# Kernel optimization log

Measured on AMD Instinct MI355X. Metric: run time of the kernel, lower is better.

## Reference

```python
import jax, jax.numpy as jnp
import numpy as np

NUM_NODES = 100000
NUM_EDGES = 1200000
DIM = 64
NUM_LAYERS = 3
NUM_GRAPHS = 512
BN_EPS = 1e-5


def setup_inputs() -> dict:
    key = jax.random.key(0)
    ks = jax.random.split(key, 12)
    x = jax.random.normal(ks[0], (NUM_NODES, DIM), dtype=jnp.float32)
    edge_index = jax.random.randint(ks[1], (2, NUM_EDGES), 0, NUM_NODES, dtype=jnp.int64)
    edge_weight = jax.random.uniform(ks[2], (NUM_EDGES,), dtype=jnp.float32)
    batch = jnp.sort(jax.random.randint(ks[3], (NUM_NODES,), 0, NUM_GRAPHS, dtype=jnp.int64))
    W1 = jax.random.normal(ks[4], (NUM_LAYERS, DIM, DIM), dtype=jnp.float32) * 0.1
    b1 = jax.random.normal(ks[5], (NUM_LAYERS, DIM), dtype=jnp.float32) * 0.1
    W2 = jax.random.normal(ks[6], (NUM_LAYERS, DIM, DIM), dtype=jnp.float32) * 0.1
    b2 = jax.random.normal(ks[7], (NUM_LAYERS, DIM), dtype=jnp.float32) * 0.1
    gamma = jax.random.uniform(ks[8], (NUM_LAYERS, DIM), dtype=jnp.float32) + 0.5
    beta = jax.random.normal(ks[9], (NUM_LAYERS, DIM), dtype=jnp.float32) * 0.1
    return {"x": x, "edge_index": edge_index, "edge_weight": edge_weight,
            "batch": batch, "pool": 0, "W1": W1, "b1": b1, "W2": W2,
            "b2": b2, "gamma": gamma, "beta": beta}


def reference(x, edge_index, edge_weight, batch, pool, W1, b1, W2, b2, gamma, beta):
    # WGINConv (eps=0): h = MLP(x + scatter_add(edge_weight * x[src] -> dst))
    # then ReLU, then BatchNorm1d in training mode (batch statistics).
    src, dst = edge_index[0], edge_index[1]
    n_nodes = x.shape[0]
    xs = []
    for i in range(W1.shape[0]):
        msg = x[src] * edge_weight[:, None]                       # [E, D] gather
        agg = jax.ops.segment_sum(msg, dst, num_segments=n_nodes)  # [N, D] scatter-add
        h = agg + x                                                # (1+eps)*x, eps=0
        h = jax.nn.relu(h @ W1[i].T + b1[i]) @ W2[i].T + b2[i]     # GIN MLP
        h = jax.nn.relu(h)
        mu = h.mean(0)
        var = ((h - mu) ** 2).mean(0)                              # biased var (BN train)
        x = gamma[i] * (h - mu) * jax.lax.rsqrt(var + BN_EPS) + beta[i]
        xs.append(x)
    if pool == 0:  # 'add' pooling (static python int)
        xpool = [jax.ops.segment_sum(v, batch, num_segments=NUM_GRAPHS) for v in xs]
    else:          # 'mean' pooling
        counts = jax.ops.segment_sum(jnp.ones((n_nodes,), x.dtype), batch,
                                     num_segments=NUM_GRAPHS)
        denom = jnp.maximum(counts, 1.0)[:, None]
        xpool = [jax.ops.segment_sum(v, batch, num_segments=NUM_GRAPHS) / denom for v in xs]
    return (jnp.concatenate(xpool, axis=1), jnp.concatenate(xs, axis=1))
```

## Files before the change

kernel.cpp:

```cpp
#include <hip/hip_runtime.h>

#define N_NODES 100000
#define N_EDGES 1200000
#define DIM     64
#define N_LAYERS 3
#define N_GRAPHS 512
#define OUTD    192
#define BN_EPS  1e-5f

#define ELL_CAP 48

#define SCAN_CHUNK 1024
#define NBLK ((N_NODES + SCAN_CHUNK - 1) / SCAN_CHUNK)

#define NPB 64
#define LDS_PITCH 65
#define NLBLK ((N_NODES + NPB - 1) / NPB)

__global__ void transpose_w(const float* __restrict__ W1, const float* __restrict__ W2,
                            float* __restrict__ W1T, float* __restrict__ W2T,
                            float* __restrict__ idaff) {
    int idx = blockIdx.x * blockDim.x + threadIdx.x;
    if (idx < 128) idaff[idx] = (idx < 64) ? 1.0f : 0.0f;
    if (idx >= N_LAYERS * DIM * DIM) return;
    int l = idx >> 12;
    int r = idx & 4095;
    int j = r >> 6;
    int k = r & 63;
    int dstp = (l << 12) + k * DIM + j;
    W1T[dstp] = W1[idx];
    W2T[dstp] = W2[idx];
}

__global__ void edge_bin_ell(const int* __restrict__ src, const int* __restrict__ dst,
                             const float* __restrict__ ew,
                             int* __restrict__ cursor, int2* __restrict__ pe) {
    int e = blockIdx.x * blockDim.x + threadIdx.x;
    if (e >= N_EDGES) return;
    int t = dst[e];
    int pos = atomicAdd(&cursor[t], 1);
    if (pos < ELL_CAP)
        pe[(size_t)t * ELL_CAP + pos] = make_int2(src[e], __float_as_int(ew[e]));
}

__global__ void hist_kernel(const int* __restrict__ dst, int* __restrict__ counts) {
    int e = blockIdx.x * blockDim.x + threadIdx.x;
    if (e >= N_EDGES) return;
    atomicAdd(&counts[dst[e]], 1);
}

__global__ void scan_partial(const int* __restrict__ C, int* __restrict__ bsum) {
    __shared__ int lds[256];
    int b = blockIdx.x, t = threadIdx.x;
    int base = b * SCAN_CHUNK + t * 4;
    int s = 0;
#pragma unroll
    for (int k = 0; k < 4; ++k) {
        int i = base + k;
        if (i < N_NODES) s += C[i];
    }
    lds[t] = s;
    __syncthreads();
    for (int o = 128; o > 0; o >>= 1) {
        if (t < o) lds[t] += lds[t + o];
        __syncthreads();
    }
    if (t == 0) bsum[b] = lds[0];
}

__global__ void scan_bsum(int* __restrict__ bsum) {
    __shared__ int lds[128];
    int t = threadIdx.x;
    int v = (t < NBLK) ? bsum[t] : 0;
    lds[t] = v;
    __syncthreads();
    for (int o = 1; o < 128; o <<= 1) {
        int add = (t >= o) ? lds[t - o] : 0;
        __syncthreads();
        lds[t] += add;
        __syncthreads();
    }
    if (t < NBLK) bsum[t] = lds[t] - v;
}

__global__ void scan_final(const int* __restrict__ C, const int* __restrict__ bsum,
                           int* __restrict__ O, int* __restrict__ cursor) {
    __shared__ int lds[256];
    int b = blockIdx.x, t = threadIdx.x;
    int base = b * SCAN_CHUNK + t * 4;
    int v[4];
    int s = 0;
#pragma unroll
    for (int k = 0; k < 4; ++k) {
        int i = base + k;
        v[k] = (i < N_NODES) ? C[i] : 0;
        s += v[k];
    }
    lds[t] = s;
    __syncthreads();
    for (int o = 1; o < 256; o <<= 1) {
        int add = (t >= o) ? lds[t - o] : 0;
        __syncthreads();
        lds[t] += add;
        __syncthreads();
    }
    int off = bsum[b] + (lds[t] - s);
#pragma unroll
    for (int k = 0; k < 4; ++k) {
        int i = base + k;
        if (i < N_NODES) {
            O[i] = off;
            cursor[i] = off;
            off += v[k];
            if (i == N_NODES - 1) O[N_NODES] = off;
        }
    }
}

__global__ void edge_bin_csr(const int* __restrict__ src, const int* __restrict__ dst,
                             const float* __restrict__ ew,
                             int* __restrict__ cursor, int2* __restrict__ pe) {
    int e = blockIdx.x * blockDim.x + threadIdx.x;
    if (e >= N_EDGES) return;
    int t = dst[e];
    int pos = atomicAdd(&cursor[t], 1);
    pe[pos] = make_int2(src[e], __float_as_int(ew[e]));
}

template <bool ELL>
__global__ void __launch_bounds__(256) layer_kernel(
    const float* __restrict__ x_in, int xstride,
    const int* __restrict__ seg,
    const int2* __restrict__ pe,
    const float* __restrict__ affine ,
    const float* __restrict__ W1T, const float* __restrict__ b1,
    const float* __restrict__ W2T, const float* __restrict__ b2,
    float* __restrict__ out ,
    float* __restrict__ pstat ) {
    __shared__ float lds[NPB * LDS_PITCH];
    int t = threadIdx.x;
    int lane = t & 63;
    int wid = __builtin_amdgcn_readfirstlane(t >> 6);
    int nbase = blockIdx.x * NPB;

    float sc_in = affine[lane];
    float sh_in = affine[64 + lane];

    for (int nn = 0; nn < 16; ++nn) {
        int n = nbase + wid * 16 + nn;
        float acc = 0.0f;
        if (n < N_NODES) {
            int beg, end;
            if (ELL) { beg = n * ELL_CAP; end = beg + seg[n]; }
            else     { beg = seg[n];      end = seg[n + 1]; }
            float a0 = x_in[(size_t)n * xstride + lane];
            float a1 = 0.0f, a2 = 0.0f, a3 = 0.0f;
            float ws = 0.0f;
            int e = beg;
            for (; e + 4 <= end; e += 4) {
                int2 p0 = pe[e];
                int2 p1 = pe[e + 1];
                int2 p2 = pe[e + 2];
                int2 p3 = pe[e + 3];
                float w0 = __int_as_float(p0.y);
                float w1 = __int_as_float(p1.y);
                float w2 = __int_as_float(p2.y);
                float w3 = __int_as_float(p3.y);
                a0 = fmaf(w0, x_in[(size_t)p0.x * xstride + lane], a0);
                a1 = fmaf(w1, x_in[(size_t)p1.x * xstride + lane], a1);
                a2 = fmaf(w2, x_in[(size_t)p2.x * xstride + lane], a2);
                a3 = fmaf(w3, x_in[(size_t)p3.x * xstride + lane], a3);
                ws += (w0 + w1) + (w2 + w3);
            }
            for (; e < end; ++e) {
                int2 p = pe[e];
                float w = __int_as_float(p.y);
                a1 = fmaf(w, x_in[(size_t)p.x * xstride + lane], a1);
                ws += w;
            }
            acc = fmaf(sc_in, (a0 + a1) + (a2 + a3), sh_in * (1.0f + ws));
        }
        lds[(wid * 16 + nn) * LDS_PITCH + lane] = acc;
    }
    __syncthreads();

    float h[16];
#pragma unroll
    for (int jj = 0; jj < 16; ++jj) h[jj] = b1[wid * 16 + jj];
#pragma unroll 4
    for (int k = 0; k < DIM; ++k) {
        float xv = lds[lane * LDS_PITCH + k];
        const float* wr = W1T + k * DIM + wid * 16;
#pragma unroll
        for (int jj = 0; jj < 16; ++jj) h[jj] = fmaf(xv, wr[jj], h[jj]);
    }
#pragma unroll
    for (int jj = 0; jj < 16; ++jj) h[jj] = fmaxf(h[jj], 0.0f);
    __syncthreads();
#pragma unroll
    for (int jj = 0; jj < 16; ++jj) lds[lane * LDS_PITCH + wid * 16 + jj] = h[jj];
    __syncthreads();

    float o[16];
#pragma unroll
    for (int jj = 0; jj < 16; ++jj) o[jj] = b2[wid * 16 + jj];
#pragma unroll 4
    for (int k = 0; k < DIM; ++k) {
        float hv = lds[lane * LDS_PITCH + k];
        const float* wr = W2T + k * DIM + wid * 16;
#pragma unroll
        for (int jj = 0; jj < 16; ++jj) o[jj] = fmaf(hv, wr[jj], o[jj]);
    }
    int n = nbase + lane;
    bool valid = (n < N_NODES);
#pragma unroll
    for (int jj = 0; jj < 16; ++jj) o[jj] = fmaxf(o[jj], 0.0f);
    if (valid) {
        float* orow = out + (size_t)n * OUTD + wid * 16;
#pragma unroll
        for (int jj = 0; jj < 16; jj += 4) {
            *(float4*)(orow + jj) = make_float4(o[jj], o[jj + 1], o[jj + 2], o[jj + 3]);
        }
    }

    float my_s = 0.0f, my_q = 0.0f;
#pragma unroll
    for (int jj = 0; jj < 16; ++jj) {
        float v = valid ? o[jj] : 0.0f;
        float vs = v, vq = v * v;
#pragma unroll
        for (int m = 1; m < 64; m <<= 1) {
            vs += __shfl_xor(vs, m);
            vq += __shfl_xor(vq, m);
        }
        if (lane == jj) { my_s = vs; my_q = vq; }
    }
    if (lane < 16) {
        size_t base = (size_t)blockIdx.x * 128 + wid * 16 + lane;
        pstat[base] = my_s;
        pstat[base + 64] = my_q;
    }
}

__global__ void __launch_bounds__(256) reduce_stats(
    const float* __restrict__ pstat,
    const float* __restrict__ gamma, const float* __restrict__ beta,
    float* __restrict__ ss ) {
    __shared__ double part[16][16];
    int b = blockIdx.x;
    int t = threadIdx.x;
    int slot = t & 15;
    int g = t >> 4;
    int d = b * 8 + (slot & 7);
    int off = (slot < 8) ? 0 : 64;
    double s = 0.0;
    for (int blk = g; blk < NLBLK; blk += 16)
        s += (double)pstat[(size_t)blk * 128 + off + d];
    part[g][slot] = s;
    __syncthreads();
    if (t < 16) {
        double x = 0.0;
#pragma unroll
        for (int k = 0; k < 16; ++k) x += part[k][t];
        part[0][t] = x;
    }
    __syncthreads();
    if (t < 8) {
        int dd = b * 8 + t;
        double mu = part[0][t] / (double)N_NODES;
        double var = part[0][8 + t] / (double)N_NODES - mu * mu;
        float inv = (float)(1.0 / sqrt(var + (double)BN_EPS));
        float sc = gamma[dd] * inv;
        ss[dd] = sc;
        ss[64 + dd] = beta[dd] - (float)mu * sc;
    }
}

__global__ void bn_pool(float* __restrict__ xs,
                        const int* __restrict__ batch,
                        const float* __restrict__ ss ,
                        float* __restrict__ pooled) {
    int g = blockIdx.x;
    int part = blockIdx.y;
    int d = threadIdx.x;
    int l = d >> 6, dd = d & 63;
    float sc = ss[l * 128 + dd];
    float sh = ss[l * 128 + 64 + dd];
    int start, end;
    {
        int lo = 0, hi = N_NODES;
        while (lo < hi) { int m = (lo + hi) >> 1; if (batch[m] < g) lo = m + 1; else hi = m; }
        start = lo;
    }
    {
        int lo = start, hi = N_NODES;
        while (lo < hi) { int m = (lo + hi) >> 1; if (batch[m] <= g) lo = m + 1; else hi = m; }
        end = lo;
    }
    float acc = 0.0f;
    for (int n = start + part; n < end; n += 4) {
        float* p = xs + (size_t)n * OUTD + d;
        float v = fmaf(*p, sc, sh);
        *p = v;
        acc += v;
    }
    atomicAdd(&pooled[(size_t)g * OUTD + d], acc);
}

extern "C" void kernel_launch(void* const* d_in, const int* in_sizes, int n_in,
                              void* d_out, int out_size, void* d_ws, size_t ws_size,
                              hipStream_t stream) {
    const float* x0    = (const float*)d_in[0];
    const int*   ei    = (const int*)d_in[1];
    const float* ew    = (const float*)d_in[2];
    const int*   batch = (const int*)d_in[3];
    const float* W1    = (const float*)d_in[5];
    const float* b1    = (const float*)d_in[6];
    const float* W2    = (const float*)d_in[7];
    const float* b2    = (const float*)d_in[8];
    const float* gamma = (const float*)d_in[9];
    const float* beta  = (const float*)d_in[10];

    float* pooled = (float*)d_out;
    float* xs     = pooled + (size_t)N_GRAPHS * OUTD;

    const int* src = ei;
    const int* dst = ei + N_EDGES;

    const size_t aux_floats = (size_t)2 * N_LAYERS * DIM * DIM + 128
                            + (size_t)N_LAYERS * 128 + (size_t)NLBLK * 128;

    const size_t ell_bytes = (size_t)N_NODES * ELL_CAP * sizeof(int2)
                           + (size_t)(N_NODES + 4) * sizeof(int)
                           + aux_floats * sizeof(float);
    bool use_ell = (ws_size >= ell_bytes);

    int2*  pe;
    int*   seg;
    float* W1T;
    int*   csr_counts = nullptr;
    int*   csr_cursor = nullptr;
    int*   csr_bsum   = nullptr;

    if (use_ell) {
        pe   = (int2*)d_ws;
        seg  = (int*)(pe + (size_t)N_NODES * ELL_CAP);
        W1T  = (float*)(seg + N_NODES + 4);
    } else {
        pe   = (int2*)d_ws;
        csr_counts = (int*)(pe + N_EDGES);
        seg        = csr_counts + N_NODES + 4;
        csr_cursor = seg + N_NODES + 4;
        csr_bsum   = csr_cursor + N_NODES + 4;
        W1T  = (float*)(csr_bsum + 128);
    }
    float* W2T   = W1T + N_LAYERS * DIM * DIM;
    float* idaff = W2T + N_LAYERS * DIM * DIM;
    float* ss    = idaff + 128;
    float* pstat = ss + N_LAYERS * 128;

    transpose_w<<<(N_LAYERS * DIM * DIM + 255) / 256, 256, 0, stream>>>(
        W1, W2, W1T, W2T, idaff);

    if (use_ell) {
        hipMemsetAsync(seg, 0, (size_t)(N_NODES + 4) * sizeof(int), stream);
        edge_bin_ell<<<(N_EDGES + 255) / 256, 256, 0, stream>>>(src, dst, ew, seg, pe);
    } else {
        hipMemsetAsync(csr_counts, 0, (size_t)(N_NODES + 4) * sizeof(int), stream);
        hist_kernel<<<(N_EDGES + 255) / 256, 256, 0, stream>>>(dst, csr_counts);
        scan_partial<<<NBLK, 256, 0, stream>>>(csr_counts, csr_bsum);
        scan_bsum<<<1, 128, 0, stream>>>(csr_bsum);
        scan_final<<<NBLK, 256, 0, stream>>>(csr_counts, csr_bsum, seg, csr_cursor);
        edge_bin_csr<<<(N_EDGES + 255) / 256, 256, 0, stream>>>(src, dst, ew,
                                                                csr_cursor, pe);
    }

    for (int i = 0; i < N_LAYERS; ++i) {
        const float* xin = (i == 0) ? x0 : (xs + (size_t)(i - 1) * DIM);
        int xstride = (i == 0) ? DIM : OUTD;
        const float* affine = (i == 0) ? idaff : (ss + (size_t)(i - 1) * 128);

        if (use_ell) {
            layer_kernel<true><<<NLBLK, 256, 0, stream>>>(
                xin, xstride, seg, pe, affine,
                W1T + (size_t)i * DIM * DIM, b1 + (size_t)i * DIM,
                W2T + (size_t)i * DIM * DIM, b2 + (size_t)i * DIM,
                xs + (size_t)i * DIM, pstat);
        } else {
            layer_kernel<false><<<NLBLK, 256, 0, stream>>>(
                xin, xstride, seg, pe, affine,
                W1T + (size_t)i * DIM * DIM, b1 + (size_t)i * DIM,
                W2T + (size_t)i * DIM * DIM, b2 + (size_t)i * DIM,
                xs + (size_t)i * DIM, pstat);
        }

        reduce_stats<<<8, 256, 0, stream>>>(
            pstat, gamma + (size_t)i * DIM, beta + (size_t)i * DIM,
            ss + (size_t)i * 128);
    }

    hipMemsetAsync(pooled, 0, (size_t)N_GRAPHS * OUTD * sizeof(float), stream);
    dim3 pgrid(N_GRAPHS, 4);
    bn_pool<<<pgrid, OUTD, 0, stream>>>(xs, batch, ss, pooled);
}
```

Measured before the change: 548.8 us.

## Build CSR via two-level bucket partition with LDS atomics instead of ELL

Replaces the ELL (or global-atomic CSR) edge binning with a two-pass partition. Edges are first split into 512-node buckets using per-block LDS histograms and a scan, then each bucket is sorted into exact per-node CSR order with LDS atomics. This avoids global atomics on per-node cursors and the padded 48-slot ELL layout, which wastes memory and silently drops edges past the cap. It adds four kernels, an extra edge-sized scratch buffer, and packs the local destination into the high bits of the source index, which assumes fewer than 2^17 nodes.

After: 558.5 us. No clear change (+1.8%).

```diff
diff --git a/kernel.cpp b/kernel.cpp
--- a/kernel.cpp
+++ b/kernel.cpp
@@ -8,14 +8,15 @@
 #define OUTD    192
 #define BN_EPS  1e-5f
 
-#define ELL_CAP 48
-
-#define SCAN_CHUNK 1024
-#define NBLK ((N_NODES + SCAN_CHUNK - 1) / SCAN_CHUNK)
-
 #define NPB 64
 #define LDS_PITCH 65
 #define NLBLK ((N_NODES + NPB - 1) / NPB)
+
+#define BSHIFT 9
+#define BUCK_NODES (1 << BSHIFT)
+#define NBUK ((N_NODES + BUCK_NODES - 1) / BUCK_NODES)
+#define EPB 4096
+#define NPBLK ((N_EDGES + EPB - 1) / EPB)
 
 __global__ void transpose_w(const float* __restrict__ W1, const float* __restrict__ W2,
                             float* __restrict__ W1T, float* __restrict__ W2T,
@@ -32,102 +33,113 @@
     W2T[dstp] = W2[idx];
 }
 
-__global__ void edge_bin_ell(const int* __restrict__ src, const int* __restrict__ dst,
-                             const float* __restrict__ ew,
-                             int* __restrict__ cursor, int2* __restrict__ pe) {
-    int e = blockIdx.x * blockDim.x + threadIdx.x;
-    if (e >= N_EDGES) return;
-    int t = dst[e];
-    int pos = atomicAdd(&cursor[t], 1);
-    if (pos < ELL_CAP)
-        pe[(size_t)t * ELL_CAP + pos] = make_int2(src[e], __float_as_int(ew[e]));
-}
-
-__global__ void hist_kernel(const int* __restrict__ dst, int* __restrict__ counts) {
-    int e = blockIdx.x * blockDim.x + threadIdx.x;
-    if (e >= N_EDGES) return;
-    atomicAdd(&counts[dst[e]], 1);
-}
-
-__global__ void scan_partial(const int* __restrict__ C, int* __restrict__ bsum) {
-    __shared__ int lds[256];
+__global__ void __launch_bounds__(256) part_hist(const int* __restrict__ dst,
+                                                 int* __restrict__ hist) {
+    __shared__ int h[NBUK];
+    int t = threadIdx.x;
+    if (t < NBUK) h[t] = 0;
+    __syncthreads();
+    int base = blockIdx.x * EPB;
+    for (int i = t; i < EPB; i += 256) {
+        int e = base + i;
+        if (e < N_EDGES) atomicAdd(&h[dst[e] >> BSHIFT], 1);
+    }
+    __syncthreads();
+    if (t < NBUK) hist[blockIdx.x * NBUK + t] = h[t];
+}
+
+__global__ void __launch_bounds__(256) part_scan(const int* __restrict__ hist,
+                                                 int* __restrict__ base,
+                                                 int* __restrict__ bstart) {
+    __shared__ int tot[256];
+    int b = threadIdx.x;
+    int run = 0;
+    if (b < NBUK) {
+        for (int k = 0; k < NPBLK; ++k) {
+            base[k * NBUK + b] = run;
+            run += hist[k * NBUK + b];
+        }
+    }
+    tot[b] = (b < NBUK) ? run : 0;
+    __syncthreads();
+    int v = tot[b];
+    for (int o = 1; o < 256; o <<= 1) {
+        int add = (b >= o) ? tot[b - o] : 0;
+        __syncthreads();
+        tot[b] += add;
+        __syncthreads();
+    }
+    int excl = tot[b] - v;
+    if (b < NBUK) {
+        bstart[b] = excl;
+        for (int k = 0; k < NPBLK; ++k) base[k * NBUK + b] += excl;
+        if (b == NBUK - 1) bstart[NBUK] = excl + v;
+    }
+}
+
+__global__ void __launch_bounds__(256) part_scatter(
+        const int* __restrict__ src, const int* __restrict__ dst,
+        const float* __restrict__ ew, const int* __restrict__ base,
+        int2* __restrict__ pp) {
+    __shared__ int cur[NBUK];
+    int t = threadIdx.x;
+    if (t < NBUK) cur[t] = base[blockIdx.x * NBUK + t];
+    __syncthreads();
+    int bb = blockIdx.x * EPB;
+    for (int i = t; i < EPB; i += 256) {
+        int e = bb + i;
+        if (e < N_EDGES) {
+            int d = dst[e];
+            int bk = d >> BSHIFT;
+            int pos = atomicAdd(&cur[bk], 1);
+            int dl = d & (BUCK_NODES - 1);
+            pp[pos] = make_int2(src[e] | (dl << 17), __float_as_int(ew[e]));
+        }
+    }
+}
+
+__global__ void __launch_bounds__(256) csr_build(
+        const int2* __restrict__ pp, const int* __restrict__ bstart,
+        int* __restrict__ seg, int2* __restrict__ pe) {
+    __shared__ int cnt[BUCK_NODES];
+    __shared__ int ssum[256];
     int b = blockIdx.x, t = threadIdx.x;
-    int base = b * SCAN_CHUNK + t * 4;
-    int s = 0;
-#pragma unroll
-    for (int k = 0; k < 4; ++k) {
-        int i = base + k;
-        if (i < N_NODES) s += C[i];
-    }
-    lds[t] = s;
-    __syncthreads();
-    for (int o = 128; o > 0; o >>= 1) {
-        if (t < o) lds[t] += lds[t + o];
+    int ebeg = bstart[b], eend = bstart[b + 1];
+    cnt[t] = 0;
+    cnt[t + 256] = 0;
+    __syncthreads();
+    for (int e = ebeg + t; e < eend; e += 256)
+        atomicAdd(&cnt[pp[e].x >> 17], 1);
+    __syncthreads();
+    int c0 = cnt[2 * t], c1 = cnt[2 * t + 1];
+    int ps = c0 + c1;
+    ssum[t] = ps;
+    __syncthreads();
+    int v = ps;
+    for (int o = 1; o < 256; o <<= 1) {
+        int add = (t >= o) ? ssum[t - o] : 0;
         __syncthreads();
-    }
-    if (t == 0) bsum[b] = lds[0];
-}
-
-__global__ void scan_bsum(int* __restrict__ bsum) {
-    __shared__ int lds[128];
-    int t = threadIdx.x;
-    int v = (t < NBLK) ? bsum[t] : 0;
-    lds[t] = v;
-    __syncthreads();
-    for (int o = 1; o < 128; o <<= 1) {
-        int add = (t >= o) ? lds[t - o] : 0;
+        ssum[t] += add;
         __syncthreads();
-        lds[t] += add;
-        __syncthreads();
-    }
-    if (t < NBLK) bsum[t] = lds[t] - v;
-}
-
-__global__ void scan_final(const int* __restrict__ C, const int* __restrict__ bsum,
-                           int* __restrict__ O, int* __restrict__ cursor) {
-    __shared__ int lds[256];
-    int b = blockIdx.x, t = threadIdx.x;
-    int base = b * SCAN_CHUNK + t * 4;
-    int v[4];
-    int s = 0;
-#pragma unroll
-    for (int k = 0; k < 4; ++k) {
-        int i = base + k;
-        v[k] = (i < N_NODES) ? C[i] : 0;
-        s += v[k];
-    }
-    lds[t] = s;
-    __syncthreads();
-    for (int o = 1; o < 256; o <<= 1) {
-        int add = (t >= o) ? lds[t - o] : 0;
-        __syncthreads();
-        lds[t] += add;
-        __syncthreads();
-    }
-    int off = bsum[b] + (lds[t] - s);
-#pragma unroll
-    for (int k = 0; k < 4; ++k) {
-        int i = base + k;
-        if (i < N_NODES) {
-            O[i] = off;
-            cursor[i] = off;
-            off += v[k];
-            if (i == N_NODES - 1) O[N_NODES] = off;
-        }
-    }
-}
-
-__global__ void edge_bin_csr(const int* __restrict__ src, const int* __restrict__ dst,
-                             const float* __restrict__ ew,
-                             int* __restrict__ cursor, int2* __restrict__ pe) {
-    int e = blockIdx.x * blockDim.x + threadIdx.x;
-    if (e >= N_EDGES) return;
-    int t = dst[e];
-    int pos = atomicAdd(&cursor[t], 1);
-    pe[pos] = make_int2(src[e], __float_as_int(ew[e]));
-}
-
-template <bool ELL>
+    }
+    int excl = ssum[t] - v;
+    int o0 = ebeg + excl;
+    int o1 = o0 + c0;
+    int n0 = (b << BSHIFT) + 2 * t;
+    if (n0 < N_NODES) seg[n0] = o0;
+    if (n0 + 1 < N_NODES) seg[n0 + 1] = o1;
+    __syncthreads();
+    cnt[2 * t] = o0;
+    cnt[2 * t + 1] = o1;
+    __syncthreads();
+    for (int e = ebeg + t; e < eend; e += 256) {
+        int2 p = pp[e];
+        int pos = atomicAdd(&cnt[p.x >> 17], 1);
+        pe[pos] = make_int2(p.x & 0x1FFFF, p.y);
+    }
+    if (b == 0 && t == 0) seg[N_NODES] = N_EDGES;
+}
+
 __global__ void __launch_bounds__(256) layer_kernel(
     const float* __restrict__ x_in, int xstride,
     const int* __restrict__ seg,
@@ -150,9 +162,8 @@
         int n = nbase + wid * 16 + nn;
         float acc = 0.0f;
         if (n < N_NODES) {
-            int beg, end;
-            if (ELL) { beg = n * ELL_CAP; end = beg + seg[n]; }
-            else     { beg = seg[n];      end = seg[n + 1]; }
+            int beg = seg[n];
+            int end = seg[n + 1];
             float a0 = x_in[(size_t)n * xstride + lane];
             float a1 = 0.0f, a2 = 0.0f, a3 = 0.0f;
             float ws = 0.0f;
@@ -327,72 +338,36 @@
     const int* src = ei;
     const int* dst = ei + N_EDGES;
 
-    const size_t aux_floats = (size_t)2 * N_LAYERS * DIM * DIM + 128
-                            + (size_t)N_LAYERS * 128 + (size_t)NLBLK * 128;
-
-    const size_t ell_bytes = (size_t)N_NODES * ELL_CAP * sizeof(int2)
-                           + (size_t)(N_NODES + 4) * sizeof(int)
-                           + aux_floats * sizeof(float);
-    bool use_ell = (ws_size >= ell_bytes);
-
-    int2*  pe;
-    int*   seg;
-    float* W1T;
-    int*   csr_counts = nullptr;
-    int*   csr_cursor = nullptr;
-    int*   csr_bsum   = nullptr;
-
-    if (use_ell) {
-        pe   = (int2*)d_ws;
-        seg  = (int*)(pe + (size_t)N_NODES * ELL_CAP);
-        W1T  = (float*)(seg + N_NODES + 4);
-    } else {
-        pe   = (int2*)d_ws;
-        csr_counts = (int*)(pe + N_EDGES);
-        seg        = csr_counts + N_NODES + 4;
-        csr_cursor = seg + N_NODES + 4;
-        csr_bsum   = csr_cursor + N_NODES + 4;
-        W1T  = (float*)(csr_bsum + 128);
-    }
-    float* W2T   = W1T + N_LAYERS * DIM * DIM;
-    float* idaff = W2T + N_LAYERS * DIM * DIM;
-    float* ss    = idaff + 128;
-    float* pstat = ss + N_LAYERS * 128;
+    int2*  pe     = (int2*)d_ws;
+    int2*  pp     = pe + N_EDGES;
+    int*   seg    = (int*)(pp + N_EDGES);
+    int*   hist   = seg + N_NODES + 4;
+    int*   pbase  = hist + (size_t)NPBLK * NBUK;
+    int*   bstart = pbase + (size_t)NPBLK * NBUK;
+    float* W1T    = (float*)(bstart + NBUK + 4);
+    float* W2T    = W1T + N_LAYERS * DIM * DIM;
+    float* idaff  = W2T + N_LAYERS * DIM * DIM;
+    float* ss     = idaff + 128;
+    float* pstat  = ss + N_LAYERS * 128;
 
     transpose_w<<<(N_LAYERS * DIM * DIM + 255) / 256, 256, 0, stream>>>(
         W1, W2, W1T, W2T, idaff);
 
-    if (use_ell) {
-        hipMemsetAsync(seg, 0, (size_t)(N_NODES + 4) * sizeof(int), stream);
-        edge_bin_ell<<<(N_EDGES + 255) / 256, 256, 0, stream>>>(src, dst, ew, seg, pe);
-    } else {
-        hipMemsetAsync(csr_counts, 0, (size_t)(N_NODES + 4) * sizeof(int), stream);
-        hist_kernel<<<(N_EDGES + 255) / 256, 256, 0, stream>>>(dst, csr_counts);
-        scan_partial<<<NBLK, 256, 0, stream>>>(csr_counts, csr_bsum);
-        scan_bsum<<<1, 128, 0, stream>>>(csr_bsum);
-        scan_final<<<NBLK, 256, 0, stream>>>(csr_counts, csr_bsum, seg, csr_cursor);
-        edge_bin_csr<<<(N_EDGES + 255) / 256, 256, 0, stream>>>(src, dst, ew,
-                                                                csr_cursor, pe);
-    }
+    part_hist<<<NPBLK, 256, 0, stream>>>(dst, hist);
+    part_scan<<<1, 256, 0, stream>>>(hist, pbase, bstart);
+    part_scatter<<<NPBLK, 256, 0, stream>>>(src, dst, ew, pbase, pp);
+    csr_build<<<NBUK, 256, 0, stream>>>(pp, bstart, seg, pe);
 
     for (int i = 0; i < N_LAYERS; ++i) {
         const float* xin = (i == 0) ? x0 : (xs + (size_t)(i - 1) * DIM);
         int xstride = (i == 0) ? DIM : OUTD;
         const float* affine = (i == 0) ? idaff : (ss + (size_t)(i - 1) * 128);
 
-        if (use_ell) {
-            layer_kernel<true><<<NLBLK, 256, 0, stream>>>(
-                xin, xstride, seg, pe, affine,
-                W1T + (size_t)i * DIM * DIM, b1 + (size_t)i * DIM,
-                W2T + (size_t)i * DIM * DIM, b2 + (size_t)i * DIM,
-                xs + (size_t)i * DIM, pstat);
-        } else {
-            layer_kernel<false><<<NLBLK, 256, 0, stream>>>(
-                xin, xstride, seg, pe, affine,
-                W1T + (size_t)i * DIM * DIM, b1 + (size_t)i * DIM,
-                W2T + (size_t)i * DIM * DIM, b2 + (size_t)i * DIM,
-                xs + (size_t)i * DIM, pstat);
-        }
+        layer_kernel<<<NLBLK, 256, 0, stream>>>(
+            xin, xstride, seg, pe, affine,
+            W1T + (size_t)i * DIM * DIM, b1 + (size_t)i * DIM,
+            W2T + (size_t)i * DIM * DIM, b2 + (size_t)i * DIM,
+            xs + (size_t)i * DIM, pstat);
 
         reduce_stats<<<8, 256, 0, stream>>>(
             pstat, gamma + (size_t)i * DIM, beta + (size_t)i * DIM,
```
